# Kernel optimization log

Measured on AMD Instinct MI355X. Metric: run time of the kernel, lower is better.

Reference implementation:

```python
import jax, jax.numpy as jnp
import numpy as np

EPS = 1e-5
G, N, H, P, K = 8, 128, 64, 64, 4  # n_groups, d_state, n_heads, head_dim, conv kernel
R = H // G  # heads per group


def _rmsnorm(x, w, eps=EPS):
    return x * jax.lax.rsqrt(jnp.mean(x * x, axis=-1, keepdims=True) + eps) * w


def setup_inputs() -> dict:
    key = jax.random.key(0)
    ks = jax.random.split(key, 8)
    B, L, Dm = 2, 1024, 2048
    d_inner = 2 * Dm                      # 4096
    conv_dim = d_inner + 2 * G * N        # 6144
    proj_dim = 2 * d_inner + 2 * G * N + H  # 10304
    return {
        "hidden_states": jax.random.normal(ks[0], (B, L, Dm), jnp.float32),
        "residual": jax.random.normal(ks[1], (B, L, Dm), jnp.float32),
        "norm_w": jnp.ones((Dm,), jnp.float32),
        "in_proj_w": jax.random.normal(ks[2], (proj_dim, Dm), jnp.float32) * 0.02,
        "conv_w": jax.random.normal(ks[3], (conv_dim, K), jnp.float32) * 0.1,
        "conv_b": jnp.zeros((conv_dim,), jnp.float32),
        "A_log": jnp.log(jnp.arange(1, H + 1, dtype=jnp.float32)),
        "D_param": jnp.ones((H,), jnp.float32),
        "dt_bias": jax.random.uniform(ks[4], (H,), jnp.float32, -4.0, -1.0),
        "gate_norm_w": jnp.ones((d_inner,), jnp.float32),
        "out_proj_w": jax.random.normal(ks[5], (Dm, d_inner), jnp.float32) * 0.02,
    }


def reference(hidden_states, residual, norm_w, in_proj_w, conv_w, conv_b,
              A_log, D_param, dt_bias, gate_norm_w, out_proj_w):
    B, L, Dm = hidden_states.shape
    d_inner = 2 * Dm
    conv_dim = d_inner + 2 * G * N

    # fused residual-add RMSNorm (residual is not None branch)
    h = hidden_states + residual
    new_residual = h
    x = _rmsnorm(h, norm_w)

    # in_proj -> [z | xBC | dt]
    proj = jnp.einsum('bld,ed->ble', x, in_proj_w)
    z = proj[..., :d_inner]
    xBC = proj[..., d_inner:d_inner + conv_dim]
    dt = proj[..., d_inner + conv_dim:]            # [B, L, H]

    # causal depthwise conv1d over xBC, then SiLU
    lhs = jnp.transpose(xBC, (0, 2, 1))            # [B, C, L]
    rhs = conv_w[:, None, :]                       # [C, 1, K]
    conv = jax.lax.conv_general_dilated(
        lhs, rhs, window_strides=(1,), padding=[(K - 1, 0)],
        feature_group_count=conv_dim)
    xBC = jax.nn.silu(jnp.transpose(conv, (0, 2, 1)) + conv_b)

    xs = xBC[..., :d_inner].reshape(B, L, G, R, P)   # per-head inputs
    Bm = xBC[..., d_inner:d_inner + G * N].reshape(B, L, G, N)
    Cm = xBC[..., d_inner + G * N:].reshape(B, L, G, N)

    dt = jax.nn.softplus(dt + dt_bias)               # [B, L, H]
    A = -jnp.exp(A_log)                              # [H]
    dA = jnp.exp(dt * A).reshape(B, L, G, R)
    dtg = dt.reshape(B, L, G, R)

    # time-major for scan
    def step(hst, inp):
        dA_t, dt_t, x_t, B_t, C_t = inp            # [B,G,R], [B,G,R], [B,G,R,P], [B,G,N], [B,G,N]
        dBx = jnp.einsum('bgr,bgn,bgrp->bgrpn', dt_t, B_t, x_t)
        hst = hst * dA_t[..., None, None] + dBx    # [B,G,R,P,N]
        y_t = jnp.einsum('bgrpn,bgn->bgrp', hst, C_t)
        return hst, y_t

    tm = lambda a: jnp.moveaxis(a, 1, 0)
    h0 = jnp.zeros((B, G, R, P, N), hidden_states.dtype)
    _, ys = jax.lax.scan(step, h0, (tm(dA), tm(dtg), tm(xs), tm(Bm), tm(Cm)))
    y = jnp.moveaxis(ys, 0, 1)                     # [B, L, G, R, P]
    y = y + D_param.reshape(G, R)[None, None, :, :, None] * xs
    y = y.reshape(B, L, d_inner)

    # gated RMSNorm then out_proj
    y = _rmsnorm(y * jax.nn.silu(z), gate_norm_w)
    out = jnp.einsum('ble,de->bld', y, out_proj_w)
    return out, new_residual
```

## Files before the change

### kernel.cpp

```cpp
#include <hip/hip_runtime.h>

#define TOK 2048
#define DM 2048
#define DI 4096
#define NG 8
#define NN 128
#define PROJ_D 10304
#define PROJ_P 10496
#define CONV_D 6144
#define LSEQ 1024
#define CHUNK 64
#define NCHUNK 16

typedef unsigned short u16;
typedef __attribute__((ext_vector_type(4))) float f32x4;
typedef __attribute__((ext_vector_type(8))) short s16x8;
typedef __attribute__((ext_vector_type(4))) unsigned short u16x4;

__device__ __forceinline__ u16 f2bf(float f) {
  union { float f; unsigned u; } x; x.f = f;
  unsigned r = (x.u + 0x7FFFu + ((x.u >> 16) & 1u)) >> 16;
  return (u16)r;
}
__device__ __forceinline__ float bf2f(u16 u) {
  union { unsigned u; float f; } x; x.u = ((unsigned)u) << 16; return x.f;
}

__device__ __forceinline__ float blockReduceSum256(float s) {
  __shared__ float red[4];
  #pragma unroll
  for (int o = 32; o > 0; o >>= 1) s += __shfl_down(s, o, 64);
  int lane = threadIdx.x & 63, wid = threadIdx.x >> 6;
  if (lane == 0) red[wid] = s;
  __syncthreads();
  return red[0] + red[1] + red[2] + red[3];
}

__global__ __launch_bounds__(256) void cvt_bf16_pad(const float* __restrict__ src, u16* __restrict__ dst,
                                                    long n_src, long n_dst) {
  long i = ((long)blockIdx.x * 256 + threadIdx.x) * 4;
  if (i >= n_dst) return;
  u16x4 o;
  if (i < n_src) {
    f32x4 v = *(const f32x4*)&src[i];
    o.x = f2bf(v.x); o.y = f2bf(v.y); o.z = f2bf(v.z); o.w = f2bf(v.w);
  } else {
    o.x = 0; o.y = 0; o.z = 0; o.w = 0;
  }
  *(u16x4*)&dst[i] = o;
}

__global__ __launch_bounds__(256) void addnorm_kernel(const float* __restrict__ hs, const float* __restrict__ res,
        const float* __restrict__ w, float* __restrict__ nres, u16* __restrict__ xbf) {
  int row = blockIdx.x;
  size_t base = (size_t)row * DM;
  int tid = threadIdx.x;
  f32x4 h[2];
  float s = 0.f;
  #pragma unroll
  for (int i = 0; i < 2; i++) {
    int off = i * 1024 + tid * 4;
    f32x4 a = *(const f32x4*)&hs[base + off];
    f32x4 b = *(const f32x4*)&res[base + off];
    f32x4 v = a + b;
    h[i] = v;
    *(f32x4*)&nres[base + off] = v;
    s += v.x * v.x + v.y * v.y + v.z * v.z + v.w * v.w;
  }
  s = blockReduceSum256(s);
  float rs = rsqrtf(s * (1.f / DM) + 1e-5f);
  #pragma unroll
  for (int i = 0; i < 2; i++) {
    int off = i * 1024 + tid * 4;
    f32x4 wv = *(const f32x4*)&w[off];
    f32x4 v = h[i];
    u16x4 o;
    o.x = f2bf(v.x * rs * wv.x);
    o.y = f2bf(v.y * rs * wv.y);
    o.z = f2bf(v.z * rs * wv.z);
    o.w = f2bf(v.w * rs * wv.w);
    *(u16x4*)&xbf[base + off] = o;
  }
}

__device__ __forceinline__ void gld_lds16(const void* g, void* l) {
  __builtin_amdgcn_global_load_lds((const __attribute__((address_space(1))) void*)g,
                                   (__attribute__((address_space(3))) void*)l, 16, 0, 0);
}

__global__ __launch_bounds__(512, 2) void gemm8p_bf(const u16* __restrict__ A, const u16* __restrict__ Bw,
                                                    u16* __restrict__ C, int K, int Cstride, int nbx);
template <bool BF16OUT>
__global__ __launch_bounds__(512, 2) void gemm8p(const u16* __restrict__ A, const u16* __restrict__ Bw,
                                                 void* __restrict__ Cv, int K, int Cstride, int nbx,
                                                 int nks, size_t part_stride) {
  __shared__ u16 As[2][256][64];
  __shared__ u16 Bs[2][256][64];
  int tid = threadIdx.x;
  int lane = tid & 63, w = tid >> 6;
  int wr = w >> 2, wc = w & 3;
  int cpx = gridDim.x >> 3;
  int bid = blockIdx.x;
  int lb = (bid & 7) * cpx + (bid >> 3);
  int ks = lb % nks;
  int tile = lb / nks;
  int by = tile / nbx, bx = tile - by * nbx;
  int Ks = K / nks;
  int k0 = ks * Ks;
  size_t m0 = (size_t)by * 256, n0 = (size_t)bx * 256;
  const u16* Ab = A + m0 * K;
  const u16* Bb = Bw + n0 * K;

  f32x4 acc[8][4];
  #pragma unroll
  for (int i = 0; i < 8; ++i)
    #pragma unroll
    for (int j = 0; j < 4; ++j) acc[i][j] = (f32x4){0.f, 0.f, 0.f, 0.f};

  int l3 = lane >> 3;
  int colsw = ((lane & 7) ^ l3) << 3;
  int fr = lane & 15, fq = lane >> 4;
  int pc0 = (fq * 8) ^ ((fr & 7) << 3);
  int pc1 = pc0 ^ 32;

  auto S = [&](int kt, int mat, int half) {
    int d = kt & 1;
    const u16* src = mat ? Bb : Ab;
    u16* dstbase = mat ? &Bs[d][0][0] : &As[d][0][0];
    #pragma unroll
    for (int j = 0; j < 2; ++j) {
      int rb = half * 128 + (w * 2 + j) * 8;
      gld_lds16(src + (size_t)(rb + l3) * K + k0 + kt * 64 + colsw, dstbase + rb * 64);
    }
  };

  int nkt = Ks >> 6;
  S(0, 1, 0); S(0, 1, 1); S(0, 0, 0); S(0, 0, 1);
  S(1, 1, 0); S(1, 1, 1);
  asm volatile("s_waitcnt vmcnt(4)" ::: "memory");
  __builtin_amdgcn_s_barrier();

  for (int kt = 0; kt < nkt; ++kt) {
    int d = kt & 1;
    s16x8 b[4][2];
    #pragma unroll
    for (int q = 0; q < 4; ++q) {
      if (q == 0) {
        #pragma unroll
        for (int ni = 0; ni < 4; ++ni) {
          b[ni][0] = *(const s16x8*)&Bs[d][wc * 64 + ni * 16 + fr][pc0];
          b[ni][1] = *(const s16x8*)&Bs[d][wc * 64 + ni * 16 + fr][pc1];
        }
      }
      s16x8 a[2][2];
      #pragma unroll
      for (int mi = 0; mi < 2; ++mi) {
        a[mi][0] = *(const s16x8*)&As[d][wr * 128 + q * 32 + mi * 16 + fr][pc0];
        a[mi][1] = *(const s16x8*)&As[d][wr * 128 + q * 32 + mi * 16 + fr][pc1];
      }
      if (q == 0)      { if (kt + 1 < nkt) S(kt + 1, 0, 0); }
      else if (q == 1) { if (kt + 1 < nkt) S(kt + 1, 0, 1); }
      else if (q == 2) { if (kt + 2 < nkt) S(kt + 2, 1, 0); }
      else {
        if (kt + 2 < nkt) { S(kt + 2, 1, 1); asm volatile("s_waitcnt vmcnt(4)" ::: "memory"); }
        else              { asm volatile("s_waitcnt vmcnt(0)" ::: "memory"); }
      }
      __builtin_amdgcn_s_barrier();
      __builtin_amdgcn_s_setprio(1);
      #pragma unroll
      for (int mi = 0; mi < 2; ++mi)
        #pragma unroll
        for (int ni = 0; ni < 4; ++ni) {
          acc[q * 2 + mi][ni] = __builtin_amdgcn_mfma_f32_16x16x32_bf16(a[mi][0], b[ni][0], acc[q * 2 + mi][ni], 0, 0, 0);
          acc[q * 2 + mi][ni] = __builtin_amdgcn_mfma_f32_16x16x32_bf16(a[mi][1], b[ni][1], acc[q * 2 + mi][ni], 0, 0, 0);
        }
      __builtin_amdgcn_s_setprio(0);
      __builtin_amdgcn_s_barrier();
    }
  }
  size_t crow0 = m0 + wr * 128 + fq * 4;
  size_t ccol0 = n0 + wc * 64 + fr;
  if constexpr (BF16OUT) {
    u16* C = (u16*)Cv;
    #pragma unroll
    for (int mf = 0; mf < 8; ++mf)
      #pragma unroll
      for (int ni = 0; ni < 4; ++ni)
        #pragma unroll
        for (int j = 0; j < 4; ++j)
          C[(crow0 + mf * 16 + j) * Cstride + ccol0 + ni * 16] = f2bf(acc[mf][ni][j]);
  } else {
    float* C = (float*)Cv + (size_t)ks * part_stride;
    #pragma unroll
    for (int mf = 0; mf < 8; ++mf)
      #pragma unroll
      for (int ni = 0; ni < 4; ++ni)
        #pragma unroll
        for (int j = 0; j < 4; ++j)
          C[(crow0 + mf * 16 + j) * Cstride + ccol0 + ni * 16] = acc[mf][ni][j];
  }
}

__global__ __launch_bounds__(256) void reduce4_kernel(const float* __restrict__ part, float* __restrict__ out) {
  size_t i = ((size_t)blockIdx.x * 256 + threadIdx.x) * 4;
  const size_t st = (size_t)TOK * DM;
  f32x4 s = *(const f32x4*)&part[i];
  s += *(const f32x4*)&part[i + st];
  s += *(const f32x4*)&part[i + 2 * st];
  s += *(const f32x4*)&part[i + 3 * st];
  *(f32x4*)&out[i] = s;
}

__global__ __launch_bounds__(256) void conv_silu_kernel(const u16* __restrict__ proj,
        const float* __restrict__ cw, const float* __restrict__ cb, u16* __restrict__ xbc) {
  long gid = (long)blockIdx.x * 256 + threadIdx.x;
  int c4 = (int)(gid % 1536);
  long t = gid / 1536;
  int l = (int)(t & 1023);
  int c = c4 * 4;
  const u16* base = proj + (size_t)t * PROJ_P + DI + c;
  f32x4 acc = *(const f32x4*)&cb[c];
  f32x4 w0 = *(const f32x4*)&cw[(c + 0) * 4];
  f32x4 w1 = *(const f32x4*)&cw[(c + 1) * 4];
  f32x4 w2 = *(const f32x4*)&cw[(c + 2) * 4];
  f32x4 w3 = *(const f32x4*)&cw[(c + 3) * 4];
  #pragma unroll
  for (int k = 0; k < 4; k++) {
    int ls = l - 3 + k;
    if (ls >= 0) {
      u16x4 v = *(const u16x4*)(base + ((long)(k - 3)) * PROJ_P);
      acc.x = fmaf(bf2f(v.x), w0[k], acc.x);
      acc.y = fmaf(bf2f(v.y), w1[k], acc.y);
      acc.z = fmaf(bf2f(v.z), w2[k], acc.z);
      acc.w = fmaf(bf2f(v.w), w3[k], acc.w);
    }
  }
  u16x4 o;
  o.x = f2bf(acc.x / (1.f + expf(-acc.x)));
  o.y = f2bf(acc.y / (1.f + expf(-acc.y)));
  o.z = f2bf(acc.z / (1.f + expf(-acc.z)));
  o.w = f2bf(acc.w / (1.f + expf(-acc.w)));
  *(u16x4*)&xbc[(size_t)t * CONV_D + c] = o;
}

__global__ __launch_bounds__(256) void dt_kernel(const u16* __restrict__ proj, const float* __restrict__ dt_bias,
        const float* __restrict__ A_log, float* __restrict__ dtspT, float* __restrict__ dtaT) {
  int idx = blockIdx.x * 256 + threadIdx.x;
  int t = idx >> 6, hh = idx & 63;
  int b = t >> 10, l = t & 1023;
  float dtv = bf2f(proj[(size_t)t * PROJ_P + (DI + CONV_D) + hh]) + dt_bias[hh];
  float sp = (dtv > 15.f) ? dtv : log1pf(expf(dtv));
  float Ah = -expf(A_log[hh]);
  size_t o = (size_t)(b * 64 + hh) * LSEQ + l;
  dtspT[o] = sp;
  dtaT[o] = sp * Ah;
}

__global__ __launch_bounds__(512) void ssd_kernel(const u16* __restrict__ xbc, const float* __restrict__ dtsp,
        const float* __restrict__ dta, const float* __restrict__ Dp, u16* __restrict__ y) {
  int bid = blockIdx.x;
  int g = bid & 7, b = (bid >> 3) & 1, r = bid >> 4;
  int h = g * 8 + r;
  int tid = threadIdx.x;
  int w = tid >> 6, lane = tid & 63;

  __shared__ u16 Bsh[2][64][128];
  __shared__ u16 Csh[2][64][128];
  __shared__ u16 Xt[2][64][64];
  __shared__ u16 Btw[2][128][64];
  __shared__ u16 GWsh[64][64];
  __shared__ u16 Hbf[64][128];
  __shared__ float dtsh[LSEQ];
  __shared__ float Lsh[LSEQ];

  const float* dtrow = dtsp + (size_t)(b * 64 + h) * LSEQ;
  const float* dtarow = dta + (size_t)(b * 64 + h) * LSEQ;
  if (tid < 256) { f32x4 v = *(const f32x4*)&dtrow[tid * 4]; *(f32x4*)&dtsh[tid * 4] = v; }
  for (int cc = w; cc < NCHUNK; cc += 8) {
    float a = dtarow[cc * 64 + lane];
    #pragma unroll
    for (int o = 1; o < 64; o <<= 1) { float t2 = __shfl_up(a, o, 64); if (lane >= o) a += t2; }
    Lsh[cc * 64 + lane] = a;
  }
  {
    u16* hp = &Hbf[0][0];
    for (int i = tid; i < 2048; i += 512) *(u16x4*)&hp[i * 4] = (u16x4){0, 0, 0, 0};
  }
  float Dv = Dp[h];
  const u16* xb = xbc + (size_t)b * LSEQ * CONV_D;
  int swz = (lane & 7) << 3;
  __syncthreads();

  auto stage = [&](int cc, int d) {
    int t0c = cc * 64;
    int pw = w - 4, ptid = tid - 256;
    #pragma unroll
    for (int q = 0; q < 4; ++q) {
      int rowb = pw * 16 + q * 4;
      int row = rowb + (lane >> 4);
      int colb = ((lane & 15) * 8) ^ ((row & 7) << 3);
      gld_lds16(xb + (size_t)(t0c + row) * CONV_D + DI + g * 128 + colb, &Bsh[d][rowb][0]);
      gld_lds16(xb + (size_t)(t0c + row) * CONV_D + DI + NG * NN + g * 128 + colb, &Csh[d][rowb][0]);
    }
    {
      int s = ptid & 63, pq = ptid >> 6;
      const u16* xr = xb + (size_t)(t0c + s) * CONV_D + g * 512 + r * 64;
      #pragma unroll
      for (int pb = 0; pb < 4; ++pb) {
        int p0 = pb * 16 + pq * 4;
        u16x4 v = *(const u16x4*)&xr[p0];
        #pragma unroll
        for (int j = 0; j < 4; ++j) {
          int p = p0 + j;
          Xt[d][p][s ^ ((p & 7) << 3)] = v[j];
        }
      }
    }
    {
      int s = ptid & 63, nq = ptid >> 6;
      float wend = __expf(Lsh[t0c + 63] - Lsh[t0c + s]) * dtsh[t0c + s];
      const u16* br = xb + (size_t)(t0c + s) * CONV_D + DI + g * 128;
      #pragma unroll
      for (int nb = 0; nb < 8; ++nb) {
        int n0 = nb * 16 + nq * 4;
        u16x4 v = *(const u16x4*)&br[n0];
        #pragma unroll
        for (int j = 0; j < 4; ++j) {
          int n = n0 + j;
          Btw[d][n][s ^ ((n & 7) << 3)] = f2bf(bf2f(v[j]) * wend);
        }
      }
    }
  };

  if (w >= 4) stage(0, 0);
  __syncthreads();

  f32x4 hst[8];
  #pragma unroll
  for (int i = 0; i < 8; i++) hst[i] = (f32x4){0.f, 0.f, 0.f, 0.f};

  for (int c = 0; c < NCHUNK; ++c) {
    int d = c & 1;
    int t0c = c * 64;
    if (w >= 4) {
      if (c + 1 < NCHUNK) stage(c + 1, d ^ 1);
    } else {
      s16x8 aC[4];
      #pragma unroll
      for (int k = 0; k < 4; ++k)
        aC[k] = *(const s16x8*)&Csh[d][w * 16 + (lane & 15)][(k * 32 + (lane >> 4) * 8) ^ swz];
      f32x4 Gacc[4];
      #pragma unroll
      for (int st = 0; st < 4; ++st) Gacc[st] = (f32x4){0.f, 0.f, 0.f, 0.f};
      #pragma unroll
      for (int st = 0; st < 4; ++st)
        #pragma unroll
        for (int k = 0; k < 4; ++k) {
          s16x8 bB = *(const s16x8*)&Bsh[d][st * 16 + (lane & 15)][(k * 32 + (lane >> 4) * 8) ^ swz];
          Gacc[st] = __builtin_amdgcn_mfma_f32_16x16x32_bf16(aC[k], bB, Gacc[st], 0, 0, 0);
        }
      #pragma unroll
      for (int st = 0; st < 4; ++st) {
        int s = st * 16 + (lane & 15);
        float Ls = Lsh[t0c + s], dts = dtsh[t0c + s];
        #pragma unroll
        for (int j = 0; j < 4; ++j) {
          int t = w * 16 + (lane >> 4) * 4 + j;
          float wgt = (s <= t) ? __expf(Lsh[t0c + t] - Ls) * dts : 0.f;
          GWsh[t][s ^ ((t & 7) << 3)] = f2bf(Gacc[st][j] * wgt);
        }
      }
      f32x4 Yacc[4], Y2acc[4];
      #pragma unroll
      for (int pt = 0; pt < 4; ++pt) { Yacc[pt] = (f32x4){0.f,0.f,0.f,0.f}; Y2acc[pt] = (f32x4){0.f,0.f,0.f,0.f}; }
      s16x8 aGW[2];
      #pragma unroll
      for (int k = 0; k < 2; ++k)
        aGW[k] = *(const s16x8*)&GWsh[w * 16 + (lane & 15)][(k * 32 + (lane >> 4) * 8) ^ swz];
      #pragma unroll
      for (int pt = 0; pt < 4; ++pt) {
        #pragma unroll
        for (int k = 0; k < 2; ++k) {
          s16x8 bX = *(const s16x8*)&Xt[d][pt * 16 + (lane & 15)][(k * 32 + (lane >> 4) * 8) ^ swz];
          Yacc[pt] = __builtin_amdgcn_mfma_f32_16x16x32_bf16(aGW[k], bX, Yacc[pt], 0, 0, 0);
        }
        #pragma unroll
        for (int k = 0; k < 4; ++k) {
          s16x8 bH = *(const s16x8*)&Hbf[pt * 16 + (lane & 15)][(k * 32 + (lane >> 4) * 8) ^ swz];
          Y2acc[pt] = __builtin_amdgcn_mfma_f32_16x16x32_bf16(aC[k], bH, Y2acc[pt], 0, 0, 0);
        }
      }
      float el[4];
      #pragma unroll
      for (int j = 0; j < 4; ++j) el[j] = __expf(Lsh[t0c + w * 16 + (lane >> 4) * 4 + j]);
      #pragma unroll
      for (int pt = 0; pt < 4; ++pt) {
        int p = pt * 16 + (lane & 15);
        #pragma unroll
        for (int j = 0; j < 4; ++j) {
          int t = w * 16 + (lane >> 4) * 4 + j;
          float xv = bf2f(Xt[d][p][t ^ ((p & 7) << 3)]);
          float yv = Yacc[pt][j] + el[j] * Y2acc[pt][j] + Dv * xv;
          y[((size_t)b * LSEQ + t0c + t) * DI + g * 512 + r * 64 + p] = f2bf(yv);
        }
      }
      float e63 = __expf(Lsh[t0c + 63]);
      s16x8 aX[2];
      #pragma unroll
      for (int k = 0; k < 2; ++k)
        aX[k] = *(const s16x8*)&Xt[d][w * 16 + (lane & 15)][(k * 32 + (lane >> 4) * 8) ^ swz];
      #pragma unroll
      for (int nt = 0; nt < 8; ++nt) {
        #pragma unroll
        for (int j = 0; j < 4; ++j) hst[nt][j] *= e63;
        #pragma unroll
        for (int k = 0; k < 2; ++k) {
          s16x8 bW = *(const s16x8*)&Btw[d][nt * 16 + (lane & 15)][(k * 32 + (lane >> 4) * 8) ^ swz];
          hst[nt] = __builtin_amdgcn_mfma_f32_16x16x32_bf16(aX[k], bW, hst[nt], 0, 0, 0);
        }
      }
    }
    __syncthreads();
    if (w < 4) {
      #pragma unroll
      for (int nt = 0; nt < 8; ++nt) {
        int n = nt * 16 + (lane & 15);
        #pragma unroll
        for (int j = 0; j < 4; ++j) {
          int p = w * 16 + (lane >> 4) * 4 + j;
          Hbf[p][n ^ ((p & 7) << 3)] = f2bf(hst[nt][j]);
        }
      }
    }
    __syncthreads();
  }
}

__global__ __launch_bounds__(256) void gate_kernel(const u16* __restrict__ y, const u16* __restrict__ proj,
        const float* __restrict__ gw, u16* __restrict__ y2) {
  int row = blockIdx.x;
  const u16* yr = y + (size_t)row * DI;
  const u16* zr = proj + (size_t)row * PROJ_P;
  int tid = threadIdx.x;
  f32x4 v[4];
  float s = 0.f;
  #pragma unroll
  for (int i = 0; i < 4; i++) {
    int off = i * 1024 + tid * 4;
    u16x4 av = *(const u16x4*)&yr[off];
    u16x4 zv = *(const u16x4*)&zr[off];
    f32x4 t;
    float z0 = bf2f(zv.x), z1 = bf2f(zv.y), z2 = bf2f(zv.z), z3 = bf2f(zv.w);
    t.x = bf2f(av.x) * (z0 / (1.f + expf(-z0)));
    t.y = bf2f(av.y) * (z1 / (1.f + expf(-z1)));
    t.z = bf2f(av.z) * (z2 / (1.f + expf(-z2)));
    t.w = bf2f(av.w) * (z3 / (1.f + expf(-z3)));
    v[i] = t;
    s += t.x * t.x + t.y * t.y + t.z * t.z + t.w * t.w;
  }
  s = blockReduceSum256(s);
  float rs = rsqrtf(s * (1.f / DI) + 1e-5f);
  #pragma unroll
  for (int i = 0; i < 4; i++) {
    int off = i * 1024 + tid * 4;
    f32x4 wv = *(const f32x4*)&gw[off];
    u16x4 o;
    o.x = f2bf(v[i].x * rs * wv.x);
    o.y = f2bf(v[i].y * rs * wv.y);
    o.z = f2bf(v[i].z * rs * wv.z);
    o.w = f2bf(v[i].w * rs * wv.w);
    *(u16x4*)&y2[(size_t)row * DI + off] = o;
  }
}

extern "C" void kernel_launch(void* const* d_in, const int* in_sizes, int n_in,
                              void* d_out, int out_size, void* d_ws, size_t ws_size,
                              hipStream_t stream) {
  (void)in_sizes; (void)n_in; (void)out_size; (void)ws_size;
  const float* hs      = (const float*)d_in[0];
  const float* res     = (const float*)d_in[1];
  const float* norm_w  = (const float*)d_in[2];
  const float* w_in    = (const float*)d_in[3];
  const float* conv_w  = (const float*)d_in[4];
  const float* conv_b  = (const float*)d_in[5];
  const float* A_log   = (const float*)d_in[6];
  const float* D_param = (const float*)d_in[7];
  const float* dt_bias = (const float*)d_in[8];
  const float* gate_w  = (const float*)d_in[9];
  const float* w_out   = (const float*)d_in[10];

  float* out  = (float*)d_out;
  float* nres = out + (size_t)TOK * DM;

  char* ws = (char*)d_ws;
  size_t off = 0;
  u16*   WB1  = (u16*)(ws + off);   off += (size_t)PROJ_P * DM * 2;
  u16*   WB2  = (u16*)(ws + off);   off += (size_t)DM * DI * 2;
  u16*   XBF  = (u16*)(ws + off);   off += (size_t)TOK * DM * 2;
  u16*   PROJ = (u16*)(ws + off);   off += (size_t)TOK * PROJ_P * 2;
  u16*   XBC  = (u16*)(ws + off);   off += (size_t)TOK * CONV_D * 2;
  float* DTSP = (float*)(ws + off); off += (size_t)TOK * 64 * 4;
  float* DTA  = (float*)(ws + off); off += (size_t)TOK * 64 * 4;
  u16*   Y    = (u16*)(ws + off);   off += (size_t)TOK * DI * 2;
  u16*   Y2   = (u16*)(ws + off);   off += (size_t)TOK * DI * 2;
  float* PART = (float*)(ws + off); off += (size_t)4 * TOK * DM * 4;

  cvt_bf16_pad<<<20992, 256, 0, stream>>>(w_in, WB1, (long)PROJ_D * DM, (long)PROJ_P * DM);
  cvt_bf16_pad<<<8192, 256, 0, stream>>>(w_out, WB2, (long)DM * DI, (long)DM * DI);
  addnorm_kernel<<<TOK, 256, 0, stream>>>(hs, res, norm_w, nres, XBF);
  gemm8p<true><<<(TOK / 256) * (PROJ_P / 256), 512, 0, stream>>>(XBF, WB1, PROJ, DM, PROJ_P, PROJ_P / 256, 1, 0);
  conv_silu_kernel<<<(TOK * (CONV_D / 4)) / 256, 256, 0, stream>>>(PROJ, conv_w, conv_b, XBC);
  dt_kernel<<<(TOK * 64) / 256, 256, 0, stream>>>(PROJ, dt_bias, A_log, DTSP, DTA);
  ssd_kernel<<<128, 512, 0, stream>>>(XBC, DTSP, DTA, D_param, Y);
  gate_kernel<<<TOK, 256, 0, stream>>>(Y, PROJ, gate_w, Y2);
  gemm8p<false><<<(TOK / 256) * (DM / 256) * 4, 512, 0, stream>>>(Y2, WB2, PART, DI, DM, DM / 256, 4, (size_t)TOK * DM);
  reduce4_kernel<<<(TOK * DM) / 1024, 256, 0, stream>>>(PART, out);
}
```

Before: 325.7 us.

## Split SSD scan across head_dim halves to double block count

Each SSD block now handles 32 of the 64 head-dim columns for one (batch, group, head), which doubles the grid from 128 to 256 blocks. The state update is re-tiled so each warp owns a 32-wide slice of d_state rather than a slice of head_dim. This aims to fill more compute units on a device where the scan was undersubscribed. The cost is that the C·B^T Gram matrix, the decay weighting and the B/C staging are recomputed redundantly in both halves.

```diff
diff --git a/kernel.cpp b/kernel.cpp
--- a/kernel.cpp
+++ b/kernel.cpp
@@ -88,8 +88,6 @@
                                    (__attribute__((address_space(3))) void*)l, 16, 0, 0);
 }
 
-__global__ __launch_bounds__(512, 2) void gemm8p_bf(const u16* __restrict__ A, const u16* __restrict__ Bw,
-                                                    u16* __restrict__ C, int K, int Cstride, int nbx);
 template <bool BF16OUT>
 __global__ __launch_bounds__(512, 2) void gemm8p(const u16* __restrict__ A, const u16* __restrict__ Bw,
                                                  void* __restrict__ Cv, int K, int Cstride, int nbx,
@@ -259,17 +257,18 @@
 __global__ __launch_bounds__(512) void ssd_kernel(const u16* __restrict__ xbc, const float* __restrict__ dtsp,
         const float* __restrict__ dta, const float* __restrict__ Dp, u16* __restrict__ y) {
   int bid = blockIdx.x;
-  int g = bid & 7, b = (bid >> 3) & 1, r = bid >> 4;
+  int g = bid & 7, b = (bid >> 3) & 1, r = (bid >> 4) & 7, ph = bid >> 7;
   int h = g * 8 + r;
+  int p0 = ph * 32;
   int tid = threadIdx.x;
   int w = tid >> 6, lane = tid & 63;
 
   __shared__ u16 Bsh[2][64][128];
   __shared__ u16 Csh[2][64][128];
-  __shared__ u16 Xt[2][64][64];
+  __shared__ u16 Xt[2][32][64];
   __shared__ u16 Btw[2][128][64];
   __shared__ u16 GWsh[64][64];
-  __shared__ u16 Hbf[64][128];
+  __shared__ u16 Hbf[32][128];
   __shared__ float dtsh[LSEQ];
   __shared__ float Lsh[LSEQ];
 
@@ -284,7 +283,7 @@
   }
   {
     u16* hp = &Hbf[0][0];
-    for (int i = tid; i < 2048; i += 512) *(u16x4*)&hp[i * 4] = (u16x4){0, 0, 0, 0};
+    for (int i = tid; i < 1024; i += 512) *(u16x4*)&hp[i * 4] = (u16x4){0, 0, 0, 0};
   }
   float Dv = Dp[h];
   const u16* xb = xbc + (size_t)b * LSEQ * CONV_D;
@@ -304,14 +303,14 @@
     }
     {
       int s = ptid & 63, pq = ptid >> 6;
-      const u16* xr = xb + (size_t)(t0c + s) * CONV_D + g * 512 + r * 64;
-      #pragma unroll
-      for (int pb = 0; pb < 4; ++pb) {
-        int p0 = pb * 16 + pq * 4;
-        u16x4 v = *(const u16x4*)&xr[p0];
+      const u16* xr = xb + (size_t)(t0c + s) * CONV_D + g * 512 + r * 64 + p0;
+      #pragma unroll
+      for (int pb = 0; pb < 2; ++pb) {
+        int pl0 = pb * 16 + pq * 4;
+        u16x4 v = *(const u16x4*)&xr[pl0];
         #pragma unroll
         for (int j = 0; j < 4; ++j) {
-          int p = p0 + j;
+          int p = pl0 + j;
           Xt[d][p][s ^ ((p & 7) << 3)] = v[j];
         }
       }
@@ -336,9 +335,11 @@
   if (w >= 4) stage(0, 0);
   __syncthreads();
 
-  f32x4 hst[8];
-  #pragma unroll
-  for (int i = 0; i < 8; i++) hst[i] = (f32x4){0.f, 0.f, 0.f, 0.f};
+  f32x4 hst[2][2];
+  #pragma unroll
+  for (int i = 0; i < 2; ++i)
+    #pragma unroll
+    for (int j = 0; j < 2; ++j) hst[i][j] = (f32x4){0.f, 0.f, 0.f, 0.f};
 
   for (int c = 0; c < NCHUNK; ++c) {
     int d = c & 1;
@@ -371,15 +372,15 @@
           GWsh[t][s ^ ((t & 7) << 3)] = f2bf(Gacc[st][j] * wgt);
         }
       }
-      f32x4 Yacc[4], Y2acc[4];
-      #pragma unroll
-      for (int pt = 0; pt < 4; ++pt) { Yacc[pt] = (f32x4){0.f,0.f,0.f,0.f}; Y2acc[pt] = (f32x4){0.f,0.f,0.f,0.f}; }
+      f32x4 Yacc[2], Y2acc[2];
+      #pragma unroll
+      for (int pt = 0; pt < 2; ++pt) { Yacc[pt] = (f32x4){0.f,0.f,0.f,0.f}; Y2acc[pt] = (f32x4){0.f,0.f,0.f,0.f}; }
       s16x8 aGW[2];
       #pragma unroll
       for (int k = 0; k < 2; ++k)
         aGW[k] = *(const s16x8*)&GWsh[w * 16 + (lane & 15)][(k * 32 + (lane >> 4) * 8) ^ swz];
       #pragma unroll
-      for (int pt = 0; pt < 4; ++pt) {
+      for (int pt = 0; pt < 2; ++pt) {
         #pragma unroll
         for (int k = 0; k < 2; ++k) {
           s16x8 bX = *(const s16x8*)&Xt[d][pt * 16 + (lane & 15)][(k * 32 + (lane >> 4) * 8) ^ swz];
@@ -395,43 +396,49 @@
       #pragma unroll
       for (int j = 0; j < 4; ++j) el[j] = __expf(Lsh[t0c + w * 16 + (lane >> 4) * 4 + j]);
       #pragma unroll
-      for (int pt = 0; pt < 4; ++pt) {
+      for (int pt = 0; pt < 2; ++pt) {
         int p = pt * 16 + (lane & 15);
         #pragma unroll
         for (int j = 0; j < 4; ++j) {
           int t = w * 16 + (lane >> 4) * 4 + j;
           float xv = bf2f(Xt[d][p][t ^ ((p & 7) << 3)]);
           float yv = Yacc[pt][j] + el[j] * Y2acc[pt][j] + Dv * xv;
-          y[((size_t)b * LSEQ + t0c + t) * DI + g * 512 + r * 64 + p] = f2bf(yv);
+          y[((size_t)b * LSEQ + t0c + t) * DI + g * 512 + r * 64 + p0 + p] = f2bf(yv);
         }
       }
       float e63 = __expf(Lsh[t0c + 63]);
-      s16x8 aX[2];
-      #pragma unroll
-      for (int k = 0; k < 2; ++k)
-        aX[k] = *(const s16x8*)&Xt[d][w * 16 + (lane & 15)][(k * 32 + (lane >> 4) * 8) ^ swz];
-      #pragma unroll
-      for (int nt = 0; nt < 8; ++nt) {
-        #pragma unroll
-        for (int j = 0; j < 4; ++j) hst[nt][j] *= e63;
-        #pragma unroll
-        for (int k = 0; k < 2; ++k) {
-          s16x8 bW = *(const s16x8*)&Btw[d][nt * 16 + (lane & 15)][(k * 32 + (lane >> 4) * 8) ^ swz];
-          hst[nt] = __builtin_amdgcn_mfma_f32_16x16x32_bf16(aX[k], bW, hst[nt], 0, 0, 0);
-        }
-      }
+      s16x8 aX[2][2];
+      #pragma unroll
+      for (int mp = 0; mp < 2; ++mp)
+        #pragma unroll
+        for (int k = 0; k < 2; ++k)
+          aX[mp][k] = *(const s16x8*)&Xt[d][mp * 16 + (lane & 15)][(k * 32 + (lane >> 4) * 8) ^ swz];
+      #pragma unroll
+      for (int mp = 0; mp < 2; ++mp)
+        #pragma unroll
+        for (int nn = 0; nn < 2; ++nn) {
+          #pragma unroll
+          for (int j = 0; j < 4; ++j) hst[mp][nn][j] *= e63;
+          #pragma unroll
+          for (int k = 0; k < 2; ++k) {
+            s16x8 bW = *(const s16x8*)&Btw[d][w * 32 + nn * 16 + (lane & 15)][(k * 32 + (lane >> 4) * 8) ^ swz];
+            hst[mp][nn] = __builtin_amdgcn_mfma_f32_16x16x32_bf16(aX[mp][k], bW, hst[mp][nn], 0, 0, 0);
+          }
+        }
     }
     __syncthreads();
     if (w < 4) {
       #pragma unroll
-      for (int nt = 0; nt < 8; ++nt) {
-        int n = nt * 16 + (lane & 15);
-        #pragma unroll
-        for (int j = 0; j < 4; ++j) {
-          int p = w * 16 + (lane >> 4) * 4 + j;
-          Hbf[p][n ^ ((p & 7) << 3)] = f2bf(hst[nt][j]);
-        }
-      }
+      for (int mp = 0; mp < 2; ++mp)
+        #pragma unroll
+        for (int nn = 0; nn < 2; ++nn) {
+          int n = w * 32 + nn * 16 + (lane & 15);
+          #pragma unroll
+          for (int j = 0; j < 4; ++j) {
+            int p = mp * 16 + (lane >> 4) * 4 + j;
+            Hbf[p][n ^ ((p & 7) << 3)] = f2bf(hst[mp][nn][j]);
+          }
+        }
     }
     __syncthreads();
   }
@@ -512,7 +519,7 @@
   gemm8p<true><<<(TOK / 256) * (PROJ_P / 256), 512, 0, stream>>>(XBF, WB1, PROJ, DM, PROJ_P, PROJ_P / 256, 1, 0);
   conv_silu_kernel<<<(TOK * (CONV_D / 4)) / 256, 256, 0, stream>>>(PROJ, conv_w, conv_b, XBC);
   dt_kernel<<<(TOK * 64) / 256, 256, 0, stream>>>(PROJ, dt_bias, A_log, DTSP, DTA);
-  ssd_kernel<<<128, 512, 0, stream>>>(XBC, DTSP, DTA, D_param, Y);
+  ssd_kernel<<<256, 512, 0, stream>>>(XBC, DTSP, DTA, D_param, Y);
   gate_kernel<<<TOK, 256, 0, stream>>>(Y, PROJ, gate_w, Y2);
   gemm8p<false><<<(TOK / 256) * (DM / 256) * 4, 512, 0, stream>>>(Y2, WB2, PART, DI, DM, DM / 256, 4, (size_t)TOK * DM);
   reduce4_kernel<<<(TOK * DM) / 1024, 256, 0, stream>>>(PART, out);
```

Result: faster. 305.6 us (-6.2%).
